# Kernel optimization log

Hardware: AMD Instinct MI355X
Metric: run time of the kernel (lower is better)

Reference implementation:

```python
import jax, jax.numpy as jnp
import numpy as np
from itertools import product

N_VOX = 100000
GRID = 128
KS = 3
K = KS ** 3
INC_MAX, OUTC_MAX = 64, 96
RUNTIME_INC, RUNTIME_OUTC = 48, 64


def _build_rulebook(rng):
    flat = rng.choice(GRID ** 3, size=N_VOX, replace=False).astype(np.int64)
    coords = np.stack(np.unravel_index(flat, (GRID, GRID, GRID)), axis=1)  # [N,3]
    # Dense lookup table: flat coord -> voxel index (or -1).
    table = np.full(GRID ** 3, -1, dtype=np.int32)
    table[flat] = np.arange(N_VOX, dtype=np.int32)
    offsets = np.array(list(product([-1, 0, 1], repeat=3)), dtype=np.int64)  # [27,3]
    idx = np.empty((K, N_VOX), dtype=np.int32)
    for k, off in enumerate(offsets):
        nb = coords + off  # stride=1, dilation=1
        valid = np.all((nb >= 0) & (nb < GRID), axis=1)
        nb_flat = (nb[:, 0] * GRID + nb[:, 1]) * GRID + nb[:, 2]
        nb_flat = np.where(valid, nb_flat, 0)
        idx[k] = np.where(valid, table[nb_flat], -1)
    return idx


def setup_inputs() -> dict:
    key = jax.random.key(0)
    kf, kw = jax.random.split(key)
    features = jax.random.normal(kf, (N_VOX, RUNTIME_INC), dtype=jnp.float32)
    # Full kernel param [K, inc_max, outc_max]; runtime-sliced inside reference.
    std = 1.0 / np.sqrt(INC_MAX * K)
    kernel = jax.random.uniform(kw, (K, INC_MAX, OUTC_MAX), dtype=jnp.float32,
                                minval=-std, maxval=std)
    idx = jnp.asarray(_build_rulebook(np.random.default_rng(0)))  # [K, N]
    return {"features": features, "kernel": kernel, "idx": idx,
            "runtime_inc": RUNTIME_INC, "runtime_outc": RUNTIME_OUTC}


def reference(features, kernel, idx, runtime_inc, runtime_outc):
    # Dynamic channel slicing (static Python ints -> jit friendly).
    w = kernel[:, :runtime_inc, :runtime_outc]          # [K, Ci, Co]
    mask = idx >= 0                                      # [K, N]
    safe = jnp.where(mask, idx, 0)
    # Gather -> per-offset GEMM -> accumulate (scatter is identity: out idx == n).
    gathered = features[safe] * mask[..., None].astype(features.dtype)  # [K, N, Ci]
    out = jnp.einsum('knc,kco->no', gathered, w)         # [N, Co]
    return out
```

## Files before the change

### kernel.cpp

```cpp
#include <hip/hip_runtime.h>
#include <hip/hip_bf16.h>


#define NVOX       100000
#define INC        48
#define INC_MAX    64
#define OUTC       64
#define OUTC_MAX   96
#define KOFF       27
#define FEAT_ROW   64
#define FEATB_ELEMS ((NVOX + 1) * FEAT_ROW)
#define WTB_K      3072
#define WTB_ELEMS  (KOFF * WTB_K)
#define WS_NEED    ((size_t)(FEATB_ELEMS + WTB_ELEMS) * 2)
#define FEAT_THREADS ((NVOX + 1) * 8)
#define FEAT_PREP_BLKS ((FEAT_THREADS + 255) / 256)
#define WTB_PREP_BLKS  (WTB_ELEMS / 256)
#define MAIN_BLOCKS 782

typedef __attribute__((ext_vector_type(8)))  short short8;
typedef __attribute__((ext_vector_type(4)))  float floatx4;
typedef __attribute__((ext_vector_type(16))) float floatx16;

__device__ __forceinline__ short f2bf(float f) {
    union { __hip_bfloat16 h; short s; } u;
    u.h = __float2bfloat16(f);
    return u.s;
}

__global__ void __launch_bounds__(256)
prep_cvt(const float* __restrict__ feat, const float* __restrict__ wk,
         short* __restrict__ featb, short* __restrict__ wtb)
{
    int b = blockIdx.x;
    if (b < FEAT_PREP_BLKS) {
        int t = b * 256 + threadIdx.x;
        if (t < FEAT_THREADS) {
            int g = t >> 3, c8 = (t & 7) * 8;
            short8 p = (short8){0, 0, 0, 0, 0, 0, 0, 0};
            if (g < NVOX && c8 < INC) {
                const floatx4* src = (const floatx4*)(feat + g * INC + c8);
                floatx4 f0 = src[0], f1 = src[1];
                #pragma unroll
                for (int j = 0; j < 4; ++j) { p[j] = f2bf(f0[j]); p[4 + j] = f2bf(f1[j]); }
            }
            *(short8*)(featb + g * FEAT_ROW + c8) = p;
        }
    } else {
        int t = (b - FEAT_PREP_BLKS) * 256 + threadIdx.x;
        int k = t / WTB_K, r = t % WTB_K;
        int chunk = r >> 3, j = r & 7;
        int f = chunk >> 6, lane = chunk & 63;
        int ks = f >> 1, nt = f & 1;
        int c = ks * 16 + (lane >> 5) * 8 + j;
        int o = nt * 32 + (lane & 31);
        wtb[t] = f2bf(wk[k * (INC_MAX * OUTC_MAX) + c * OUTC_MAX + o]);
    }
}

__global__ void __launch_bounds__(256, 3)
spconv_main(const short* __restrict__ featb, const short* __restrict__ wtb,
            const int* __restrict__ idx, float* __restrict__ out)
{
    __shared__ short Bs[4][WTB_K];

    const int tid  = threadIdx.x;
    const int lane = tid & 63;
    const int wave = tid >> 6;
    const int l32  = lane & 31;
    const int hi   = lane >> 5;

    int bid = blockIdx.x;
    int sb  = (bid < 776) ? ((bid & 7) * 97 + (bid >> 3)) : bid;

    const int m0   = (sb * 4 + wave) * 32;
    const bool act = (m0 < NVOX);
    const int rr   = act ? (m0 + l32) : 0;

    floatx16 acc[2];
    #pragma unroll
    for (int nt = 0; nt < 2; ++nt)
        #pragma unroll
        for (int r = 0; r < 16; ++r) acc[nt][r] = 0.f;

    short8 A[2][3];
    short8 bst[2][2];
    int    rowg[4];

    auto ldrow = [&](int k) {
        int t0 = idx[k * NVOX + rr];
        rowg[k & 3] = (t0 < 0) ? NVOX : t0;
    };
    auto aload = [&](int k) {
        const short* p = featb + rowg[k & 3] * FEAT_ROW + hi * 8;
        A[k & 1][0] = *(const short8*)(p);
        A[k & 1][1] = *(const short8*)(p + 16);
        A[k & 1][2] = *(const short8*)(p + 32);
    };
    auto bload = [&](int k) {
        bst[k & 1][0] = *(const short8*)(wtb + k * WTB_K + tid * 8);
        if (tid < 128)
            bst[k & 1][1] = *(const short8*)(wtb + k * WTB_K + 2048 + tid * 8);
    };
    auto compute = [&](int k) {
        #pragma unroll
        for (int ks = 0; ks < 3; ++ks) {
            short8 b0 = *(const short8*)&Bs[k & 3][(ks * 128 + lane) * 8];
            short8 b1 = *(const short8*)&Bs[k & 3][(ks * 128 + 64 + lane) * 8];
            acc[0] = __builtin_amdgcn_mfma_f32_32x32x16_bf16(
                A[k & 1][ks], b0, acc[0], 0, 0, 0);
            acc[1] = __builtin_amdgcn_mfma_f32_32x32x16_bf16(
                A[k & 1][ks], b1, acc[1], 0, 0, 0);
        }
    };

    ldrow(0); ldrow(1); ldrow(2); ldrow(3);
    bload(0); bload(1);
    aload(0); aload(1);

    #pragma unroll
    for (int j = 0; j < 14; ++j) {
        const int kk = 2 * j;

        *(short8*)&Bs[kk & 3][tid * 8] = bst[0][0];
        if (tid < 128) *(short8*)&Bs[kk & 3][2048 + tid * 8] = bst[0][1];
        if (kk + 1 < KOFF) {
            *(short8*)&Bs[(kk + 1) & 3][tid * 8] = bst[1][0];
            if (tid < 128) *(short8*)&Bs[(kk + 1) & 3][2048 + tid * 8] = bst[1][1];
        }
        __syncthreads();

        if (kk + 2 < KOFF) bload(kk + 2);
        if (kk + 3 < KOFF) bload(kk + 3);
        if (kk + 4 < KOFF) ldrow(kk + 4);
        if (kk + 5 < KOFF) ldrow(kk + 5);

        compute(kk);
        if (kk + 2 < KOFF) aload(kk + 2);
        if (kk + 1 < KOFF) {
            compute(kk + 1);
            if (kk + 3 < KOFF) aload(kk + 3);
        }
    }

    if (act) {
        #pragma unroll
        for (int nt = 0; nt < 2; ++nt) {
            #pragma unroll
            for (int r = 0; r < 16; ++r) {
                int row = (r & 3) + 8 * (r >> 2) + 4 * hi;
                out[(m0 + row) * OUTC + nt * 32 + l32] = acc[nt][r];
            }
        }
    }
}

__global__ void __launch_bounds__(256)
spconv_fallback(const float* __restrict__ feat, const float* __restrict__ wk,
                const int* __restrict__ idx, float* __restrict__ out)
{
    int t = blockIdx.x * 256 + threadIdx.x;
    if (t >= NVOX * OUTC) return;
    int n = t >> 6, o = t & 63;
    float s = 0.f;
    for (int k = 0; k < KOFF; ++k) {
        int g = idx[k * NVOX + n];
        if (g >= 0) {
            const float* fr = feat + g * INC;
            const float* wr = wk + k * (INC_MAX * OUTC_MAX) + o;
            #pragma unroll 8
            for (int c = 0; c < INC; ++c) s += fr[c] * wr[c * OUTC_MAX];
        }
    }
    out[t] = s;
}

extern "C" void kernel_launch(void* const* d_in, const int* in_sizes, int n_in,
                              void* d_out, int out_size, void* d_ws, size_t ws_size,
                              hipStream_t stream) {
    const float* feat = (const float*)d_in[0];
    const float* wk   = (const float*)d_in[1];
    const int*   idx  = (const int*)d_in[2];
    float* out = (float*)d_out;

    if (ws_size >= WS_NEED) {
        short* featb = (short*)d_ws;
        short* wtb   = featb + FEATB_ELEMS;
        prep_cvt<<<FEAT_PREP_BLKS + WTB_PREP_BLKS, 256, 0, stream>>>(feat, wk, featb, wtb);
        spconv_main<<<MAIN_BLOCKS, 256, 0, stream>>>(featb, wtb, idx, out);
    } else {
        spconv_fallback<<<(NVOX * OUTC + 255) / 256, 256, 0, stream>>>(feat, wk, idx, out);
    }
}
```

Before: 108.4 us.

## Give each wave two 32-row M tiles and halve block size to 128 threads

```diff
diff --git a/kernel.cpp b/kernel.cpp
--- a/kernel.cpp
+++ b/kernel.cpp
@@ -58,7 +58,7 @@
     }
 }
 
-__global__ void __launch_bounds__(256, 3)
+__global__ void __launch_bounds__(128, 2)
 spconv_main(const short* __restrict__ featb, const short* __restrict__ wtb,
             const int* __restrict__ idx, float* __restrict__ out)
 {
@@ -73,44 +73,58 @@
     int bid = blockIdx.x;
     int sb  = (bid < 776) ? ((bid & 7) * 97 + (bid >> 3)) : bid;
 
-    const int m0   = (sb * 4 + wave) * 32;
-    const bool act = (m0 < NVOX);
-    const int rr   = act ? (m0 + l32) : 0;
-
-    floatx16 acc[2];
+    const int m0 = sb * 128 + wave * 64;
+    const int ra = m0 + l32;
+    const int rb = m0 + 32 + l32;
+    const int rra = (ra < NVOX) ? ra : 0;
+    const int rrb = (rb < NVOX) ? rb : 0;
+
+    floatx16 acc[2][2];
     #pragma unroll
-    for (int nt = 0; nt < 2; ++nt)
-        #pragma unroll
-        for (int r = 0; r < 16; ++r) acc[nt][r] = 0.f;
-
-    short8 A[2][3];
-    short8 bst[2][2];
-    int    rowg[4];
+    for (int i = 0; i < 2; ++i)
+        #pragma unroll
+        for (int j = 0; j < 2; ++j)
+            #pragma unroll
+            for (int r = 0; r < 16; ++r) acc[i][j][r] = 0.f;
+
+    short8 A[2][2][3];
+    short8 bst[4][3];
+    int    row0[4], row1[4];
 
     auto ldrow = [&](int k) {
-        int t0 = idx[k * NVOX + rr];
-        rowg[k & 3] = (t0 < 0) ? NVOX : t0;
+        int t0 = idx[k * NVOX + rra];
+        int t1 = idx[k * NVOX + rrb];
+        row0[k & 3] = (t0 < 0) ? NVOX : t0;
+        row1[k & 3] = (t1 < 0) ? NVOX : t1;
     };
     auto aload = [&](int k) {
-        const short* p = featb + rowg[k & 3] * FEAT_ROW + hi * 8;
-        A[k & 1][0] = *(const short8*)(p);
-        A[k & 1][1] = *(const short8*)(p + 16);
-        A[k & 1][2] = *(const short8*)(p + 32);
+        const short* p0 = featb + row0[k & 3] * FEAT_ROW + hi * 8;
+        const short* p1 = featb + row1[k & 3] * FEAT_ROW + hi * 8;
+        #pragma unroll
+        for (int ks = 0; ks < 3; ++ks) {
+            A[k & 1][0][ks] = *(const short8*)(p0 + ks * 16);
+            A[k & 1][1][ks] = *(const short8*)(p1 + ks * 16);
+        }
     };
     auto bload = [&](int k) {
-        bst[k & 1][0] = *(const short8*)(wtb + k * WTB_K + tid * 8);
-        if (tid < 128)
-            bst[k & 1][1] = *(const short8*)(wtb + k * WTB_K + 2048 + tid * 8);
+        #pragma unroll
+        for (int c = 0; c < 3; ++c)
+            bst[k & 3][c] = *(const short8*)(wtb + k * WTB_K + (c * 128 + tid) * 8);
+    };
+    auto commit = [&](int k) {
+        #pragma unroll
+        for (int c = 0; c < 3; ++c)
+            *(short8*)&Bs[k & 3][(c * 128 + tid) * 8] = bst[k & 3][c];
     };
     auto compute = [&](int k) {
         #pragma unroll
         for (int ks = 0; ks < 3; ++ks) {
-            short8 b0 = *(const short8*)&Bs[k & 3][(ks * 128 + lane) * 8];
-            short8 b1 = *(const short8*)&Bs[k & 3][(ks * 128 + 64 + lane) * 8];
-            acc[0] = __builtin_amdgcn_mfma_f32_32x32x16_bf16(
-                A[k & 1][ks], b0, acc[0], 0, 0, 0);
-            acc[1] = __builtin_amdgcn_mfma_f32_32x32x16_bf16(
-                A[k & 1][ks], b1, acc[1], 0, 0, 0);
+            short8 b0 = *(const short8*)&Bs[k & 3][((ks * 2 + 0) * 64 + lane) * 8];
+            short8 b1 = *(const short8*)&Bs[k & 3][((ks * 2 + 1) * 64 + lane) * 8];
+            acc[0][0] = __builtin_amdgcn_mfma_f32_32x32x16_bf16(A[k & 1][0][ks], b0, acc[0][0], 0, 0, 0);
+            acc[0][1] = __builtin_amdgcn_mfma_f32_32x32x16_bf16(A[k & 1][0][ks], b1, acc[0][1], 0, 0, 0);
+            acc[1][0] = __builtin_amdgcn_mfma_f32_32x32x16_bf16(A[k & 1][1][ks], b0, acc[1][0], 0, 0, 0);
+            acc[1][1] = __builtin_amdgcn_mfma_f32_32x32x16_bf16(A[k & 1][1][ks], b1, acc[1][1], 0, 0, 0);
         }
     };
 
@@ -122,12 +136,8 @@
     for (int j = 0; j < 14; ++j) {
         const int kk = 2 * j;
 
-        *(short8*)&Bs[kk & 3][tid * 8] = bst[0][0];
-        if (tid < 128) *(short8*)&Bs[kk & 3][2048 + tid * 8] = bst[0][1];
-        if (kk + 1 < KOFF) {
-            *(short8*)&Bs[(kk + 1) & 3][tid * 8] = bst[1][0];
-            if (tid < 128) *(short8*)&Bs[(kk + 1) & 3][2048 + tid * 8] = bst[1][1];
-        }
+        commit(kk);
+        if (kk + 1 < KOFF) commit(kk + 1);
         __syncthreads();
 
         if (kk + 2 < KOFF) bload(kk + 2);
@@ -143,13 +153,14 @@
         }
     }
 
-    if (act) {
-        #pragma unroll
-        for (int nt = 0; nt < 2; ++nt) {
-            #pragma unroll
-            for (int r = 0; r < 16; ++r) {
-                int row = (r & 3) + 8 * (r >> 2) + 4 * hi;
-                out[(m0 + row) * OUTC + nt * 32 + l32] = acc[nt][r];
+    #pragma unroll
+    for (int mh = 0; mh < 2; ++mh) {
+        #pragma unroll
+        for (int r = 0; r < 16; ++r) {
+            int g = m0 + mh * 32 + (r & 3) + 8 * (r >> 2) + 4 * hi;
+            if (g < NVOX) {
+                out[g * OUTC + l32]      = acc[mh][0][r];
+                out[g * OUTC + 32 + l32] = acc[mh][1][r];
             }
         }
     }
@@ -187,7 +198,7 @@
         short* featb = (short*)d_ws;
         short* wtb   = featb + FEATB_ELEMS;
         prep_cvt<<<FEAT_PREP_BLKS + WTB_PREP_BLKS, 256, 0, stream>>>(feat, wk, featb, wtb);
-        spconv_main<<<MAIN_BLOCKS, 256, 0, stream>>>(featb, wtb, idx, out);
+        spconv_main<<<MAIN_BLOCKS, 128, 0, stream>>>(featb, wtb, idx, out);
     } else {
         spconv_fallback<<<(NVOX * OUTC + 255) / 256, 256, 0, stream>>>(feat, wk, idx, out);
     }
```

After: 109.6 us. Within noise of the previous version (+1.2%).
